# Optimization experiments

Measured on AMD Instinct MI355X. Metric: run time of the kernel, lower is better.

## Reference

```python
import jax, jax.numpy as jnp
import numpy as np

N, T, E, D, U = 32, 2048, 512, 1024, 256


def setup_inputs() -> dict:
    key = jax.random.key(0)
    ks = jax.random.split(key, 6)
    queries = jax.random.normal(ks[0], (N, 1, D), dtype=jnp.float32)
    prev = jax.random.uniform(ks[1], (N, T), dtype=jnp.float32)
    prev = prev / jnp.sum(prev, axis=1, keepdims=True)  # distribution-like initial alignment
    memory = jax.random.normal(ks[2], (N, T, E), dtype=jnp.float32)
    W_q = jax.random.normal(ks[3], (D, U), dtype=jnp.float32) * (1.0 / np.sqrt(D))
    W_k = jax.random.normal(ks[4], (E, U), dtype=jnp.float32) * (1.0 / np.sqrt(E))
    v = jax.random.uniform(ks[5], (U,), dtype=jnp.float32)
    return {"queries": queries, "previous_alignments": prev, "memory": memory,
            "W_q": W_q, "W_k": W_k, "v": v}


def safe_cumprod_exclusive(x):
    # exclusive cumprod via log-space cumsum, clamped like the torch original
    logsum = jnp.cumsum(jnp.log(jnp.clip(x, 1e-20, 1.0)), axis=1)  # [N,T]
    excl = jnp.concatenate([jnp.zeros_like(logsum[:, :1]), logsum], axis=1)[:, :-1]
    return jnp.exp(excl)


def reference(queries, previous_alignments, memory, W_q, W_k, v):
    # Bahdanau additive score (normalize=False path)
    proj_key = jnp.einsum('bte,eu->btu', memory, W_k)          # set_memory
    proj_q = jnp.einsum('bqd,du->bqu', queries, W_q)           # [N,1,U]
    weights = jnp.einsum('btu,u->bt', jnp.tanh(proj_q + proj_key), v)  # [N,T]
    p_choose = jax.nn.sigmoid(weights)
    # monotonic attention recursion in cumsum/cumprod form
    cumprod_1mp = safe_cumprod_exclusive(1.0 - p_choose)
    alignments = p_choose * cumprod_1mp * jnp.cumsum(
        previous_alignments / jnp.clip(cumprod_1mp, 1e-10, 1.0), axis=1)
    contexts = jnp.einsum('bt,bte->be', alignments, memory)    # bmm + squeeze
    return (contexts, alignments)
```

## Files before the change

### kernel.cpp

```cpp
#include <hip/hip_runtime.h>
#include <math.h>

#define N_ 32
#define T_ 2048
#define E_ 512
#define D_ 1024
#define U_ 256

typedef __attribute__((ext_vector_type(8))) short bf16x8;
typedef __attribute__((ext_vector_type(16))) float f32x16;

__device__ __forceinline__ short f2bf_rne(float x) {
  unsigned int u = __float_as_uint(x);
  unsigned int r = u + 0x7FFFu + ((u >> 16) & 1u);
  return (short)(r >> 16);
}
__device__ __forceinline__ short f2bf_trunc(float x) {
  return (short)(__float_as_uint(x) >> 16);
}
__device__ __forceinline__ float bf2f(short h) {
  return __uint_as_float(((unsigned int)(unsigned short)h) << 16);
}
__device__ __forceinline__ float fast_tanh(float x) {
  float t = exp2f(x * 2.8853900817779268f);
  return 1.0f - 2.0f * __builtin_amdgcn_rcpf(t + 1.0f);
}
__device__ __forceinline__ float fast_sigmoid(float w) {
  return __builtin_amdgcn_rcpf(1.0f + exp2f(-1.4426950408889634f * w));
}

__device__ __forceinline__ void gload_lds16(const float* src, void* dst) {
  __builtin_amdgcn_global_load_lds(
      (const __attribute__((address_space(1))) void*)src,
      (__attribute__((address_space(3))) void*)dst, 16, 0, 0);
}

__global__ __launch_bounds__(256) void prep_kernel(
    const float* __restrict__ Wk, const float* __restrict__ queries,
    const float* __restrict__ Wq, bf16x8* __restrict__ whiP,
    bf16x8* __restrict__ wloP, float* __restrict__ pq_part) {
  const int wg = blockIdx.x, tid = threadIdx.x;
  if (wg < 64) {
    const int fid = wg * 256 + tid;
    const int lane = fid & 63;
    const int ub = (fid >> 6) & 7;
    const int kc = (fid >> 9) & 3;
    const int c = fid >> 11;
    const int u = ub * 32 + (lane & 31);
    const int e0 = c * 64 + kc * 16 + (lane >> 5) * 8;
    bf16x8 H, L;
#pragma unroll
    for (int j = 0; j < 8; ++j) {
      float x = Wk[(size_t)(e0 + j) * U_ + u];
      short h = f2bf_trunc(x);
      H[j] = h;
      L[j] = f2bf_rne(x - bf2f(h));
    }
    whiP[fid] = H;
    wloP[fid] = L;
  } else {
    const int ch = (wg - 64) & 3;
    const int bb = (wg - 64) >> 2;
    const int d0 = ch * 256;
    const float* q = queries + bb * D_ + d0;
    const float* wq = Wq + (size_t)d0 * U_ + tid;
    float acc = 0.f;
#pragma unroll 8
    for (int d = 0; d < 256; ++d)
      acc = fmaf(q[d], wq[(size_t)d * U_], acc);
    pq_part[(bb * 4 + ch) * U_ + tid] = acc;
  }
}

__global__ __launch_bounds__(256, 2) void score_kernel(
    const float* __restrict__ memory, const bf16x8* __restrict__ whiP,
    const bf16x8* __restrict__ wloP, const float* __restrict__ pq_part,
    const float* __restrict__ v, float* __restrict__ p_choose) {
  __shared__ float sAf[2][128 * 32];
  __shared__ float smem_w[4][128];

  const int b = blockIdx.y;
  const int t0 = blockIdx.x * 128;
  const int tid = threadIdx.x;
  const int lane = tid & 63;
  const int ty = tid >> 6;
  const int l31 = lane & 31;
  const int half = lane >> 5;

  f32x16 acc[4][2];
#pragma unroll
  for (int mt = 0; mt < 4; ++mt)
#pragma unroll
    for (int nt = 0; nt < 2; ++nt)
#pragma unroll
      for (int r = 0; r < 16; ++r) acc[mt][nt][r] = 0.f;

  const float* gsrc[4];
  int ldsoff[4];
#pragma unroll
  for (int i = 0; i < 4; ++i) {
    const int C = (ty * 4 + i) * 64 + lane;
    const int r = C >> 3;
    const int sl = (C & 7) ^ (r & 7);
    gsrc[i] = memory + ((size_t)(b * T_ + t0 + r)) * E_ + sl * 4;
    ldsoff[i] = (ty * 4 + i) * 1024;
  }

  auto do_stage = [&](int buf, int itn) {
    const int co = itn * 32;
#pragma unroll
    for (int i = 0; i < 4; ++i)
      gload_lds16(gsrc[i] + co, (char*)&sAf[buf][0] + ldsoff[i]);
  };

  do_stage(0, 0);
  __syncthreads();

  for (int it = 0; it < 16; ++it) {
    if (it < 15) do_stage((it + 1) & 1, it + 1);

    const char* base = (const char*)&sAf[it & 1][0];
#pragma unroll
    for (int kc = 0; kc < 2; ++kc) {
      bf16x8 bh[2], bl[2];
#pragma unroll
      for (int nt = 0; nt < 2; ++nt) {
        const int fidx = ((it * 2 + kc) * 8 + (ty * 2 + nt)) * 64 + lane;
        bh[nt] = whiP[fidx];
        bl[nt] = wloP[fidx];
      }
      const int ls0 = half * 2 + kc * 4;
      bf16x8 ah[4], al[4];
#pragma unroll
      for (int mt = 0; mt < 4; ++mt) {
        const int m = mt * 32 + l31;
        const char* rowp = base + (size_t)m * 128;
        float4 f0 = *(const float4*)(rowp + ((ls0 ^ (m & 7)) * 16));
        float4 f1 = *(const float4*)(rowp + (((ls0 + 1) ^ (m & 7)) * 16));
        float xs[8] = {f0.x, f0.y, f0.z, f0.w, f1.x, f1.y, f1.z, f1.w};
#pragma unroll
        for (int i = 0; i < 8; ++i) {
          short h = f2bf_trunc(xs[i]);
          ah[mt][i] = h;
          al[mt][i] = f2bf_rne(xs[i] - bf2f(h));
        }
      }
#pragma unroll
      for (int mt = 0; mt < 4; ++mt)
#pragma unroll
        for (int nt = 0; nt < 2; ++nt) {
          acc[mt][nt] = __builtin_amdgcn_mfma_f32_32x32x16_bf16(ah[mt], bh[nt], acc[mt][nt], 0, 0, 0);
          acc[mt][nt] = __builtin_amdgcn_mfma_f32_32x32x16_bf16(ah[mt], bl[nt], acc[mt][nt], 0, 0, 0);
          acc[mt][nt] = __builtin_amdgcn_mfma_f32_32x32x16_bf16(al[mt], bh[nt], acc[mt][nt], 0, 0, 0);
        }
    }
    __syncthreads();
  }

  const int u0 = ty * 64 + l31;
  const int u1 = u0 + 32;
  float pq0 = 0.f, pq1 = 0.f;
#pragma unroll
  for (int c = 0; c < 4; ++c) {
    pq0 += pq_part[(b * 4 + c) * U_ + u0];
    pq1 += pq_part[(b * 4 + c) * U_ + u1];
  }
  const float v0 = v[u0], v1 = v[u1];
#pragma unroll
  for (int mt = 0; mt < 4; ++mt)
#pragma unroll
    for (int r = 0; r < 16; ++r) {
      float s = fast_tanh(acc[mt][0][r] + pq0) * v0 + fast_tanh(acc[mt][1][r] + pq1) * v1;
#pragma unroll
      for (int off = 1; off < 32; off <<= 1) s += __shfl_xor(s, off, 64);
      if (l31 == 0) {
        const int row = mt * 32 + (r & 3) + 8 * (r >> 2) + 4 * half;
        smem_w[ty][row] = s;
      }
    }
  __syncthreads();
  if (tid < 128) {
    const float w = smem_w[0][tid] + smem_w[1][tid] + smem_w[2][tid] + smem_w[3][tid];
    p_choose[b * T_ + t0 + tid] = fast_sigmoid(w);
  }
}

__device__ __forceinline__ float block_incl_scan(float val, float* sbuf, int tid) {
  float x = val;
  sbuf[tid] = x;
  __syncthreads();
#pragma unroll
  for (int off = 1; off < 256; off <<= 1) {
    float t = (tid >= off) ? sbuf[tid - off] : 0.f;
    __syncthreads();
    x += t;
    sbuf[tid] = x;
    __syncthreads();
  }
  return x;
}

__global__ __launch_bounds__(256) void scan_kernel(
    const float* __restrict__ p_choose, const float* __restrict__ prev,
    float* __restrict__ align_out, float* __restrict__ ctx_out) {
  __shared__ float sbuf[256];
  const int b = blockIdx.x, tid = threadIdx.x;
  ctx_out[b * E_ + tid] = 0.f;
  ctx_out[b * E_ + 256 + tid] = 0.f;
  const int base = b * T_ + tid * 8;
  float4 p0 = *(const float4*)(p_choose + base);
  float4 p1 = *(const float4*)(p_choose + base + 4);
  float p[8] = {p0.x, p0.y, p0.z, p0.w, p1.x, p1.y, p1.z, p1.w};
  float s[8];
  float run = 0.f;
#pragma unroll
  for (int k = 0; k < 8; ++k) {
    float x = 1.0f - p[k];
    x = fminf(fmaxf(x, 1e-20f), 1.0f);
    run += logf(x);
    s[k] = run;
  }
  float incl = block_incl_scan(run, sbuf, tid);
  float excl = incl - run;
  float cp[8];
#pragma unroll
  for (int k = 0; k < 8; ++k)
    cp[k] = expf(excl + (k ? s[k - 1] : 0.f));
  float4 r0 = *(const float4*)(prev + base);
  float4 r1 = *(const float4*)(prev + base + 4);
  float pr[8] = {r0.x, r0.y, r0.z, r0.w, r1.x, r1.y, r1.z, r1.w};
  float s2[8];
  float run2 = 0.f;
#pragma unroll
  for (int k = 0; k < 8; ++k) {
    float d = fminf(fmaxf(cp[k], 1e-10f), 1.0f);
    run2 += pr[k] / d;
    s2[k] = run2;
  }
  float incl2 = block_incl_scan(run2, sbuf, tid);
  float excl2 = incl2 - run2;
#pragma unroll
  for (int k = 0; k < 8; ++k)
    p[k] = p[k] * cp[k] * (excl2 + s2[k]);
  *(float4*)(align_out + base) = make_float4(p[0], p[1], p[2], p[3]);
  *(float4*)(align_out + base + 4) = make_float4(p[4], p[5], p[6], p[7]);
}

__global__ __launch_bounds__(256) void ctx_kernel(
    const float* __restrict__ memory, const float* __restrict__ align,
    float* __restrict__ ctx_out) {
  const int wg = blockIdx.x, tid = threadIdx.x;
  const int b = wg >> 4;
  const int t0 = (wg & 15) * 128 + (tid >> 7) * 64;
  const int col = (tid & 127) * 4;
  const float* mrow = memory + ((size_t)(b * T_ + t0)) * E_ + col;
  const float* arow = align + b * T_ + t0;
  float4 a = make_float4(0.f, 0.f, 0.f, 0.f);
  for (int t = 0; t < 64; t += 4) {
    float4 m0 = *(const float4*)(mrow + (size_t)(t + 0) * E_);
    float4 m1 = *(const float4*)(mrow + (size_t)(t + 1) * E_);
    float4 m2 = *(const float4*)(mrow + (size_t)(t + 2) * E_);
    float4 m3 = *(const float4*)(mrow + (size_t)(t + 3) * E_);
    float a0 = arow[t], a1 = arow[t + 1], a2 = arow[t + 2], a3 = arow[t + 3];
    a.x = fmaf(a0, m0.x, a.x); a.y = fmaf(a0, m0.y, a.y);
    a.z = fmaf(a0, m0.z, a.z); a.w = fmaf(a0, m0.w, a.w);
    a.x = fmaf(a1, m1.x, a.x); a.y = fmaf(a1, m1.y, a.y);
    a.z = fmaf(a1, m1.z, a.z); a.w = fmaf(a1, m1.w, a.w);
    a.x = fmaf(a2, m2.x, a.x); a.y = fmaf(a2, m2.y, a.y);
    a.z = fmaf(a2, m2.z, a.z); a.w = fmaf(a2, m2.w, a.w);
    a.x = fmaf(a3, m3.x, a.x); a.y = fmaf(a3, m3.y, a.y);
    a.z = fmaf(a3, m3.z, a.z); a.w = fmaf(a3, m3.w, a.w);
  }
  float* dst = ctx_out + b * E_ + col;
  atomicAdd(dst + 0, a.x);
  atomicAdd(dst + 1, a.y);
  atomicAdd(dst + 2, a.z);
  atomicAdd(dst + 3, a.w);
}

extern "C" void kernel_launch(void* const* d_in, const int* in_sizes, int n_in,
                              void* d_out, int out_size, void* d_ws, size_t ws_size,
                              hipStream_t stream) {
  (void)in_sizes; (void)n_in; (void)out_size; (void)ws_size;
  const float* queries = (const float*)d_in[0];
  const float* prev    = (const float*)d_in[1];
  const float* memory  = (const float*)d_in[2];
  const float* Wq      = (const float*)d_in[3];
  const float* Wk      = (const float*)d_in[4];
  const float* v       = (const float*)d_in[5];

  float* out = (float*)d_out;
  float* ctx_out = out;
  float* align_out = out + N_ * E_;

  float* ws = (float*)d_ws;
  bf16x8* whiP    = (bf16x8*)ws;
  bf16x8* wloP    = (bf16x8*)(ws + 65536);
  float* p_choose = ws + 131072;
  float* pq_part  = ws + 196608;

  prep_kernel<<<dim3(64 + 128), 256, 0, stream>>>(Wk, queries, Wq, whiP, wloP, pq_part);
  score_kernel<<<dim3(T_ / 128, N_), 256, 0, stream>>>(memory, whiP, wloP, pq_part, v, p_choose);
  scan_kernel<<<dim3(N_), 256, 0, stream>>>(p_choose, prev, align_out, ctx_out);
  ctx_kernel<<<dim3(512), 256, 0, stream>>>(memory, align_out, ctx_out);
}
```

Measured before the change: 272.5 us.

## Remap score GEMM so each wave owns full U columns for its rows

Changes the wave-to-tile mapping in the score kernel. Each wave now handles 32 time rows across all 256 U columns (8 N-tiles) instead of all 128 rows across 64 columns. Each A element is therefore read from LDS and split into bf16 hi/lo once per wave rather than being redundantly converted by all four waves. The tanh-v reduction also completes inside a wave, which removes the shared-memory cross-wave sum and its barrier. In exchange, every wave streams all of the pre-packed W_k fragments from global memory, a 4x increase in B-operand loads per block, though these are likely cache-resident.

```diff
diff --git a/kernel.cpp b/kernel.cpp
--- a/kernel.cpp
+++ b/kernel.cpp
@@ -77,7 +77,6 @@
     const bf16x8* __restrict__ wloP, const float* __restrict__ pq_part,
     const float* __restrict__ v, float* __restrict__ p_choose) {
   __shared__ float sAf[2][128 * 32];
-  __shared__ float smem_w[4][128];
 
   const int b = blockIdx.y;
   const int t0 = blockIdx.x * 128;
@@ -87,13 +86,11 @@
   const int l31 = lane & 31;
   const int half = lane >> 5;
 
-  f32x16 acc[4][2];
-#pragma unroll
-  for (int mt = 0; mt < 4; ++mt)
-#pragma unroll
-    for (int nt = 0; nt < 2; ++nt)
-#pragma unroll
-      for (int r = 0; r < 16; ++r) acc[mt][nt][r] = 0.f;
+  f32x16 acc[8];
+#pragma unroll
+  for (int nt = 0; nt < 8; ++nt)
+#pragma unroll
+    for (int r = 0; r < 16; ++r) acc[nt][r] = 0.f;
 
   const float* gsrc[4];
   int ldsoff[4];
@@ -116,72 +113,63 @@
   do_stage(0, 0);
   __syncthreads();
 
+  const int m = ty * 32 + l31;
+  const int msw = m & 7;
+
   for (int it = 0; it < 16; ++it) {
     if (it < 15) do_stage((it + 1) & 1, it + 1);
 
     const char* base = (const char*)&sAf[it & 1][0];
+    const char* rowp = base + (size_t)m * 128;
 #pragma unroll
     for (int kc = 0; kc < 2; ++kc) {
-      bf16x8 bh[2], bl[2];
-#pragma unroll
-      for (int nt = 0; nt < 2; ++nt) {
-        const int fidx = ((it * 2 + kc) * 8 + (ty * 2 + nt)) * 64 + lane;
-        bh[nt] = whiP[fidx];
-        bl[nt] = wloP[fidx];
+      const int ls0 = half * 2 + kc * 4;
+      float4 f0 = *(const float4*)(rowp + ((ls0 ^ msw) * 16));
+      float4 f1 = *(const float4*)(rowp + (((ls0 + 1) ^ msw) * 16));
+      float xs[8] = {f0.x, f0.y, f0.z, f0.w, f1.x, f1.y, f1.z, f1.w};
+      bf16x8 ah, al;
+#pragma unroll
+      for (int i = 0; i < 8; ++i) {
+        short h = f2bf_trunc(xs[i]);
+        ah[i] = h;
+        al[i] = f2bf_rne(xs[i] - bf2f(h));
       }
-      const int ls0 = half * 2 + kc * 4;
-      bf16x8 ah[4], al[4];
-#pragma unroll
-      for (int mt = 0; mt < 4; ++mt) {
-        const int m = mt * 32 + l31;
-        const char* rowp = base + (size_t)m * 128;
-        float4 f0 = *(const float4*)(rowp + ((ls0 ^ (m & 7)) * 16));
-        float4 f1 = *(const float4*)(rowp + (((ls0 + 1) ^ (m & 7)) * 16));
-        float xs[8] = {f0.x, f0.y, f0.z, f0.w, f1.x, f1.y, f1.z, f1.w};
-#pragma unroll
-        for (int i = 0; i < 8; ++i) {
-          short h = f2bf_trunc(xs[i]);
-          ah[mt][i] = h;
-          al[mt][i] = f2bf_rne(xs[i] - bf2f(h));
-        }
+      const bf16x8* bhp = whiP + (size_t)((it * 2 + kc) * 8) * 64 + lane;
+      const bf16x8* blp = wloP + (size_t)((it * 2 + kc) * 8) * 64 + lane;
+#pragma unroll
+      for (int nt = 0; nt < 8; ++nt) {
+        bf16x8 bh = bhp[nt * 64];
+        bf16x8 bl = blp[nt * 64];
+        acc[nt] = __builtin_amdgcn_mfma_f32_32x32x16_bf16(ah, bh, acc[nt], 0, 0, 0);
+        acc[nt] = __builtin_amdgcn_mfma_f32_32x32x16_bf16(ah, bl, acc[nt], 0, 0, 0);
+        acc[nt] = __builtin_amdgcn_mfma_f32_32x32x16_bf16(al, bh, acc[nt], 0, 0, 0);
       }
-#pragma unroll
-      for (int mt = 0; mt < 4; ++mt)
-#pragma unroll
-        for (int nt = 0; nt < 2; ++nt) {
-          acc[mt][nt] = __builtin_amdgcn_mfma_f32_32x32x16_bf16(ah[mt], bh[nt], acc[mt][nt], 0, 0, 0);
-          acc[mt][nt] = __builtin_amdgcn_mfma_f32_32x32x16_bf16(ah[mt], bl[nt], acc[mt][nt], 0, 0, 0);
-          acc[mt][nt] = __builtin_amdgcn_mfma_f32_32x32x16_bf16(al[mt], bh[nt], acc[mt][nt], 0, 0, 0);
-        }
     }
     __syncthreads();
   }
 
-  const int u0 = ty * 64 + l31;
-  const int u1 = u0 + 32;
-  float pq0 = 0.f, pq1 = 0.f;
-#pragma unroll
-  for (int c = 0; c < 4; ++c) {
-    pq0 += pq_part[(b * 4 + c) * U_ + u0];
-    pq1 += pq_part[(b * 4 + c) * U_ + u1];
-  }
-  const float v0 = v[u0], v1 = v[u1];
-#pragma unroll
-  for (int mt = 0; mt < 4; ++mt)
-#pragma unroll
-    for (int r = 0; r < 16; ++r) {
-      float s = fast_tanh(acc[mt][0][r] + pq0) * v0 + fast_tanh(acc[mt][1][r] + pq1) * v1;
-#pragma unroll
-      for (int off = 1; off < 32; off <<= 1) s += __shfl_xor(s, off, 64);
-      if (l31 == 0) {
-        const int row = mt * 32 + (r & 3) + 8 * (r >> 2) + 4 * half;
-        smem_w[ty][row] = s;
-      }
+  float pq[8], vv[8];
+#pragma unroll
+  for (int nt = 0; nt < 8; ++nt) {
+    const int u = nt * 32 + l31;
+    float s = 0.f;
+#pragma unroll
+    for (int c = 0; c < 4; ++c) s += pq_part[(b * 4 + c) * U_ + u];
+    pq[nt] = s;
+    vv[nt] = v[u];
+  }
+#pragma unroll
+  for (int r = 0; r < 16; ++r) {
+    float s = 0.f;
+#pragma unroll
+    for (int nt = 0; nt < 8; ++nt)
+      s += fast_tanh(acc[nt][r] + pq[nt]) * vv[nt];
+#pragma unroll
+    for (int off = 1; off < 32; off <<= 1) s += __shfl_xor(s, off, 64);
+    if (l31 == 0) {
+      const int row = ty * 32 + (r & 3) + 8 * (r >> 2) + 4 * half;
+      p_choose[b * T_ + t0 + row] = fast_sigmoid(s);
     }
-  __syncthreads();
-  if (tid < 128) {
-    const float w = smem_w[0][tid] + smem_w[1][tid] + smem_w[2][tid] + smem_w[3][tid];
-    p_choose[b * T_ + t0 + tid] = fast_sigmoid(w);
   }
 }
 
```

Result: no change. 275.0 us (+0.9%).
